# Kernel tuning notes

Measured on AMD Instinct MI355X. Metric: run time of the kernel, lower is better.

Reference implementation:

```python
import jax, jax.numpy as jnp
import numpy as np

# Model hyperparameters (from init_kwargs)
SIG = 10.0      # kernel length scale 'sig'
C = 0.0         # energy integration constant 'c'
STD = 1.0       # data std 'std'
N_ATOMS = 21    # aspirin-like molecule
T_ROWS = 12000  # n_train * n_perms (permutation-expanded training rows)
DESC = N_ATOMS * (N_ATOMS - 1) // 2  # 210
BATCH = 64


def setup_inputs() -> dict:
    key = jax.random.key(0)
    k1, k2, k3 = jax.random.split(key, 3)
    # Geometries: M x N x 3 Cartesian coordinates (spread out so atoms are distinct)
    Rs = jax.random.normal(k1, (BATCH, N_ATOMS, 3), dtype=jnp.float32) * 2.0
    # Permutation-expanded training descriptors (inverse distances -> positive)
    xs_train = jax.random.uniform(k2, (T_ROWS, DESC), dtype=jnp.float32, minval=0.05, maxval=1.0)
    Jx_alphas = jax.random.normal(k3, (T_ROWS, DESC), dtype=jnp.float32)
    return {"Rs": Rs, "xs_train": xs_train, "Jx_alphas": Jx_alphas}


def reference(Rs, xs_train, Jx_alphas):
    sig = SIG
    q = np.sqrt(5.0) / sig
    M, N, _ = Rs.shape
    i, j = np.tril_indices(N, k=-1)

    # Pairwise atomic displacement vectors and distances. Diagonal is padded with 1
    # (instead of inf as in the torch code) -- every diagonal contribution below is
    # multiplied by an exact zero (expand_tril zeroes the diagonal, diffs diag = 0),
    # so the value is irrelevant but this keeps gradients finite.
    diffs = Rs[:, :, None, :] - Rs[:, None, :, :]          # [M, N, N, 3]
    eye = jnp.eye(N, dtype=Rs.dtype)
    dists = jnp.sqrt(jnp.sum(diffs * diffs, axis=-1) + eye)  # [M, N, N]

    # Inverse-distance descriptor (strict lower triangle)
    xs = 1.0 / dists[:, i, j]                              # [M, DESC]

    # Descriptor-space differences vs all (permuted) training points
    x_diffs = (q * xs)[:, None, :] - q * xs_train[None]    # [M, T, DESC]
    x_dists = jnp.sqrt(jnp.sum(x_diffs * x_diffs, axis=-1))  # [M, T]

    # Matern-5/2 kernel pieces
    exp_xs = (5.0 / (3.0 * sig * sig)) * jnp.exp(-x_dists)   # [M, T]
    dot_x_diff_Jx = jnp.einsum('mtd,td->mt', x_diffs, Jx_alphas)  # [M, T]
    exp_xs_1_x_dists = exp_xs * (1.0 + x_dists)              # [M, T]

    # Descriptor-space force pieces
    F1s_x = jnp.einsum('mt,mtd->md', exp_xs * dot_x_diff_Jx, x_diffs)  # [M, DESC]
    F2s_x = exp_xs_1_x_dists @ Jx_alphas                               # [M, DESC]
    Fs_x = (F1s_x - F2s_x) * STD

    # expand_tril: scatter descriptor-space forces into symmetric NxN with zero diag
    full = jnp.zeros((M, N, N), dtype=Rs.dtype)
    full = full.at[:, i, j].set(Fs_x).at[:, j, i].set(Fs_x)

    # Cartesian forces: sum over first atom index (torch's .sum(dim=1))
    Fs = jnp.einsum('mab,mabk->mbk', full / dists ** 3, diffs)  # [M, N, 3]

    # Energies
    Es = jnp.sum(exp_xs_1_x_dists * dot_x_diff_Jx, axis=-1) / q
    Es = C + Es * STD
    return Es, Fs
```

## Files before the change

### kernel.cpp

```cpp
#include <hip/hip_runtime.h>
#include <hip/hip_fp16.h>
#include <math.h>

#define N_ATOMS 21
#define DESC 210
#define APAD 224
#define T_ROWS 12000
#define BATCH 64
#define NBLK_A 376
#define PCW 216

#define QCONST 0.22360679774997896f
#define K0CONST (1.0f/60.0f)

typedef short bf16x8 __attribute__((ext_vector_type(8)));
typedef float f32x4 __attribute__((ext_vector_type(4)));

__device__ __forceinline__ float u2f(unsigned int u) {
    union { unsigned int u; float f; } x; x.u = u; return x.f;
}
__device__ __forceinline__ unsigned short f2bf(float f) {
    union { float f; unsigned int u; } x; x.f = f;
    unsigned int r = x.u + 0x7fffu + ((x.u >> 16) & 1u);
    return (unsigned short)(r >> 16);
}
__device__ __forceinline__ float bf2f(unsigned short h) {
    return u2f((unsigned int)h << 16);
}

__global__ __launch_bounds__(256) void k_prep(const float* __restrict__ Rs,
                                              unsigned short* __restrict__ Abf,
                                              float* __restrict__ na2) {
    int m = blockIdx.x;
    __shared__ float R[N_ATOMS * 3];
    __shared__ float red[256];
    int tid = threadIdx.x;
    if (tid < N_ATOMS * 3) R[tid] = Rs[m * N_ATOMS * 3 + tid];
    __syncthreads();
    float val = 0.f;
    if (tid < DESC) {
        int p = tid;
        int i = (int)((1.0f + sqrtf(1.0f + 8.0f * (float)p)) * 0.5f);
        while (i * (i - 1) / 2 > p) --i;
        while ((i + 1) * i / 2 <= p) ++i;
        int j = p - i * (i - 1) / 2;
        float dx = R[i * 3 + 0] - R[j * 3 + 0];
        float dy = R[i * 3 + 1] - R[j * 3 + 1];
        float dz = R[i * 3 + 2] - R[j * 3 + 2];
        float d = sqrtf(dx * dx + dy * dy + dz * dz);
        val = QCONST / d;
    }
    unsigned short h = f2bf(val);
    if (tid < APAD) Abf[m * APAD + tid] = h;
    float va = bf2f(h);
    red[tid] = va * va;
    __syncthreads();
    for (int s = 128; s > 0; s >>= 1) {
        if (tid < s) red[tid] += red[tid + s];
        __syncthreads();
    }
    if (tid == 0) na2[m] = red[0];
}

#define BS_OFF 0
#define JS_OFF 14848
#define XT_OFF 29696
#define W_OFF  61952
#define NB_OFF 71168
#define BJ_OFF 71296
#define NA_OFF 71424
#define LDS_SZ 71680

__global__ __launch_bounds__(256) void k_fused(const float* __restrict__ Btr,
                                               const float* __restrict__ Jx,
                                               const unsigned short* __restrict__ Abf,
                                               const float* __restrict__ na2,
                                               float* __restrict__ es_p,
                                               float* __restrict__ rs_p,
                                               __half* __restrict__ pC) {
    __shared__ char lds[LDS_SZ];
    const int blk = blockIdx.x;
    const int t0 = blk * 32;
    const int tid = threadIdx.x;
    const int lane = tid & 63;
    const int w = __builtin_amdgcn_readfirstlane(tid >> 6);
    const int lr = lane & 15;
    const int kb = lane >> 4;

    uint4 au[7];
    {
        const unsigned short* ap = Abf + (w * 16 + lr) * APAD + kb * 8;
#pragma unroll
        for (int k8 = 0; k8 < 7; k8++) au[k8] = *(const uint4*)(ap + k8 * 32);
    }
    if (tid < 64) *(float*)(lds + NA_OFF + tid * 4) = na2[tid];

    {
        const int g = tid >> 3, gl = tid & 7;
        int tr = t0 + g; if (tr > T_ROWS - 1) tr = T_ROWS - 1;
        const float* bp = Btr + (size_t)tr * DESC;
        const float* jp = Jx + (size_t)tr * DESC;
        float nb = 0.f, bj = 0.f;
#pragma unroll
        for (int it = 0; it < 15; it++) {
            int c = it * 8 + gl;
            if (c < 116) {
                float2 vb = make_float2(0.f, 0.f), vj = make_float2(0.f, 0.f);
                if (c < 105) {
                    vb = *(const float2*)(bp + 2 * c);
                    vj = *(const float2*)(jp + 2 * c);
                }
                unsigned short hbx = f2bf(vb.x), hby = f2bf(vb.y);
                unsigned short hjx = f2bf(vj.x), hjy = f2bf(vj.y);
                *(unsigned int*)(lds + BS_OFF + g * 464 + c * 4) = (unsigned)hbx | ((unsigned)hby << 16);
                *(unsigned int*)(lds + JS_OFF + g * 464 + c * 4) = (unsigned)hjx | ((unsigned)hjy << 16);
                if (c < 112) {
                    const int d = 2 * c;
                    *(unsigned short*)(lds + XT_OFF + d * 144 + g * 2) = hbx;
                    *(unsigned short*)(lds + XT_OFF + (d + 1) * 144 + g * 2) = hby;
                    *(unsigned short*)(lds + XT_OFF + d * 144 + 64 + g * 2) = hjx;
                    *(unsigned short*)(lds + XT_OFF + (d + 1) * 144 + 64 + g * 2) = hjy;
                }
                float fbx = bf2f(hbx), fby = bf2f(hby);
                float fjx = bf2f(hjx), fjy = bf2f(hjy);
                nb = fmaf(fbx, fbx, nb); nb = fmaf(fby, fby, nb);
                bj = fmaf(fbx, fjx, bj); bj = fmaf(fby, fjy, bj);
            }
        }
#pragma unroll
        for (int m = 1; m < 8; m <<= 1) { nb += __shfl_xor(nb, m); bj += __shfl_xor(bj, m); }
        if (gl == 0) {
            *(float*)(lds + NB_OFF + g * 4) = nb;
            *(float*)(lds + BJ_OFF + g * 4) = bj;
        }
    }
    __syncthreads();

    f32x4 accP[2] = {{0.f,0.f,0.f,0.f},{0.f,0.f,0.f,0.f}};
    f32x4 accQ[2] = {{0.f,0.f,0.f,0.f},{0.f,0.f,0.f,0.f}};
#pragma unroll
    for (int k8 = 0; k8 < 7; k8++) {
        union { uint4 u; bf16x8 h; } a;
        a.u = au[k8];
#pragma unroll
        for (int nt = 0; nt < 2; nt++) {
            union { uint4 u; bf16x8 h; } bu, ju;
            const int ro = (nt * 16 + lr) * 464 + k8 * 64 + kb * 16;
            bu.u = *(const uint4*)(lds + BS_OFF + ro);
            ju.u = *(const uint4*)(lds + JS_OFF + ro);
            accP[nt] = __builtin_amdgcn_mfma_f32_16x16x32_bf16(a.h, bu.h, accP[nt], 0, 0, 0);
            accQ[nt] = __builtin_amdgcn_mfma_f32_16x16x32_bf16(a.h, ju.h, accQ[nt], 0, 0, 0);
        }
    }

    float na4[4];
#pragma unroll
    for (int r = 0; r < 4; r++)
        na4[r] = *(const float*)(lds + NA_OFF + (w * 16 + kb * 4 + r) * 4);
    float es4[4] = {0.f,0.f,0.f,0.f}, rs4[4] = {0.f,0.f,0.f,0.f};
#pragma unroll
    for (int nt = 0; nt < 2; nt++) {
        const int row = nt * 16 + lr;
        const float nb_c = *(const float*)(lds + NB_OFF + row * 4);
        const float bj_c = *(const float*)(lds + BJ_OFF + row * 4);
        const float msk = (t0 + row < T_ROWS) ? 1.f : 0.f;
#pragma unroll
        for (int r = 0; r < 4; r++) {
            float S = na4[r] + QCONST * QCONST * nb_c - 2.f * QCONST * accP[nt][r];
            float xd = sqrtf(fmaxf(S, 0.f));
            float e = K0CONST * __expf(-xd);
            float dot = (accQ[nt][r] - QCONST * bj_c) * msk;
            float w1 = e * dot;
            float w2 = e * (1.f + xd) * msk;
            es4[r] += w2 * dot; rs4[r] += w1;
            const int mrow = w * 16 + kb * 4 + r;
            *(unsigned short*)(lds + W_OFF + mrow * 144 + row * 2) = f2bf(QCONST * w1);
            *(unsigned short*)(lds + W_OFF + mrow * 144 + 64 + row * 2) = f2bf(w2);
        }
    }
#pragma unroll
    for (int m = 1; m < 16; m <<= 1) {
#pragma unroll
        for (int r = 0; r < 4; r++) {
            es4[r] += __shfl_xor(es4[r], m);
            rs4[r] += __shfl_xor(rs4[r], m);
        }
    }
    if (lr == 0) {
#pragma unroll
        for (int r = 0; r < 4; r++) {
            es_p[(size_t)(w * 16 + kb * 4 + r) * NBLK_A + blk] = es4[r];
            rs_p[(size_t)(w * 16 + kb * 4 + r) * NBLK_A + blk] = rs4[r];
        }
    }
    __syncthreads();

    {
        union { uint4 u; bf16x8 h; } wa0, wa1;
        const char* Wp = lds + W_OFF + (w * 16 + lr) * 144;
        wa0.u = *(const uint4*)(Wp + kb * 16);
        wa1.u = *(const uint4*)(Wp + 64 + kb * 16);
        __half* D = (__half*)lds;
#pragma unroll
        for (int dt = 0; dt < 14; dt++) {
            union { uint4 u; bf16x8 h; } xb0, xb1;
            const char* Xp = lds + XT_OFF + (dt * 16 + lr) * 144;
            xb0.u = *(const uint4*)(Xp + kb * 16);
            xb1.u = *(const uint4*)(Xp + 64 + kb * 16);
            f32x4 acc = {0.f, 0.f, 0.f, 0.f};
            acc = __builtin_amdgcn_mfma_f32_16x16x32_bf16(wa0.h, xb0.h, acc, 0, 0, 0);
            acc = __builtin_amdgcn_mfma_f32_16x16x32_bf16(wa1.h, xb1.h, acc, 0, 0, 0);
#pragma unroll
            for (int r = 0; r < 4; r++)
                D[(w * 16 + kb * 4 + r) * 224 + dt * 16 + lr] = __float2half(acc[r]);
        }
    }
    __syncthreads();

    {
        const char* D = (const char*)lds;
        for (int i = tid; i < 64 * 27; i += 256) {
            const int mrow = i / 27, oct = i % 27;
            uint4 v = *(const uint4*)(D + mrow * 448 + oct * 16);
            *(uint4*)((char*)pC + (((size_t)mrow * NBLK_A + blk) * PCW + oct * 8) * 2) = v;
        }
    }
}

__global__ __launch_bounds__(256) void k_final(const float* __restrict__ Rs,
                                               const unsigned short* __restrict__ Abf,
                                               const float* __restrict__ es_p,
                                               const float* __restrict__ rs_p,
                                               const __half* __restrict__ pC,
                                               float* __restrict__ out) {
    const int m = blockIdx.x;
    const int tid = threadIdx.x;
    __shared__ float parts[27][8][8];
    __shared__ float fsx[DESC];
    __shared__ float R[N_ATOMS * 3];
    __shared__ float s_rs, s_es;
    if (tid < N_ATOMS * 3) R[tid] = Rs[m * N_ATOMS * 3 + tid];
    if (tid < 216) {
        const int cg = tid / 27, o = tid % 27;
        float facc[8];
#pragma unroll
        for (int e = 0; e < 8; e++) facc[e] = 0.f;
        const __half* base = pC + (size_t)m * NBLK_A * PCW + o * 8;
#pragma unroll 4
        for (int c = cg; c < NBLK_A; c += 8) {
            uint4 v = *(const uint4*)(base + (size_t)c * PCW);
            const __half2* h = (const __half2*)&v;
#pragma unroll
            for (int p2 = 0; p2 < 4; p2++) {
                float2 f = __half22float2(h[p2]);
                facc[p2 * 2] += f.x;
                facc[p2 * 2 + 1] += f.y;
            }
        }
#pragma unroll
        for (int e = 0; e < 8; e++) parts[o][cg][e] = facc[e];
    }
    __syncthreads();
    if (tid < 64) {
        float es = 0.f, rs = 0.f;
        for (int c2 = tid; c2 < NBLK_A; c2 += 64) {
            es += es_p[(size_t)m * NBLK_A + c2];
            rs += rs_p[(size_t)m * NBLK_A + c2];
        }
        for (int mask = 1; mask < 64; mask <<= 1) {
            es += __shfl_xor(es, mask);
            rs += __shfl_xor(rs, mask);
        }
        if (tid == 0) { s_es = es; s_rs = rs; }
    }
    __syncthreads();
    if (tid < DESC) {
        float s = 0.f;
        const int o = tid >> 3, e = tid & 7;
#pragma unroll
        for (int cg = 0; cg < 8; cg++) s += parts[o][cg][e];
        fsx[tid] = s_rs * bf2f(Abf[m * APAD + tid]) - s;
    }
    if (tid == 0) out[m] = s_es * (1.0f / QCONST);
    __syncthreads();
    if (tid < N_ATOMS * 3) {
        int b = tid / 3, kk = tid % 3;
        float acc = 0.f;
        for (int a = 0; a < N_ATOMS; a++) {
            if (a == b) continue;
            float dx = R[a * 3 + 0] - R[b * 3 + 0];
            float dy = R[a * 3 + 1] - R[b * 3 + 1];
            float dz = R[a * 3 + 2] - R[b * 3 + 2];
            float d2 = dx * dx + dy * dy + dz * dz;
            float dist = sqrtf(d2);
            float inv3 = 1.0f / (d2 * dist);
            int hi = (a > b) ? a : b, lo = (a > b) ? b : a;
            int p = hi * (hi - 1) / 2 + lo;
            float diffk = (kk == 0) ? dx : ((kk == 1) ? dy : dz);
            acc = fmaf(fsx[p] * inv3, diffk, acc);
        }
        out[BATCH + m * N_ATOMS * 3 + tid] = acc;
    }
}

extern "C" void kernel_launch(void* const* d_in, const int* in_sizes, int n_in,
                              void* d_out, int out_size, void* d_ws, size_t ws_size,
                              hipStream_t stream) {
    (void)in_sizes; (void)n_in; (void)out_size; (void)ws_size;
    const float* Rs = (const float*)d_in[0];
    const float* Btr = (const float*)d_in[1];
    const float* Jx = (const float*)d_in[2];
    float* out = (float*)d_out;

    char* ws = (char*)d_ws;
    unsigned short* Abf = (unsigned short*)ws;  ws += (size_t)BATCH * APAD * 2;
    float* na2 = (float*)ws;                    ws += BATCH * 4;
    float* es_p = (float*)ws;                   ws += (size_t)BATCH * NBLK_A * 4;
    float* rs_p = (float*)ws;                   ws += (size_t)BATCH * NBLK_A * 4;
    __half* pC = (__half*)ws;

    k_prep<<<dim3(BATCH), dim3(256), 0, stream>>>(Rs, Abf, na2);
    k_fused<<<dim3(NBLK_A), dim3(256), 0, stream>>>(Btr, Jx, Abf, na2, es_p, rs_p, pC);
    k_final<<<dim3(BATCH), dim3(256), 0, stream>>>(Rs, Abf, es_p, rs_p, pC, out);
}
```

Before: 36.82 us.

## Use 24-row tiles over 500 blocks with batched loads and wider final reduction

Each block now handles 24 training rows instead of 32, so 12000 rows split evenly into 500 blocks with no tail masking. Global loads are issued as batched register arrays and split across threads by array (B vs J) before conversion. The norm and dot precomputation moves to a separate pass that reads back from LDS. The padded tile rows and columns are zeroed explicitly. The final reduction kernel uses 512 threads, with a separate warp summing the energy partials in parallel. More blocks give better CU coverage, but the MFMA padding wastes 8 of every 32 rows and there are more partials to reduce.

```diff
diff --git a/kernel.cpp b/kernel.cpp
--- a/kernel.cpp
+++ b/kernel.cpp
@@ -7,7 +7,8 @@
 #define APAD 224
 #define T_ROWS 12000
 #define BATCH 64
-#define NBLK_A 376
+#define NBLK 500
+#define TROWS_B 24
 #define PCW 216
 
 #define QCONST 0.22360679774997896f
@@ -80,61 +81,96 @@
                                                __half* __restrict__ pC) {
     __shared__ char lds[LDS_SZ];
     const int blk = blockIdx.x;
-    const int t0 = blk * 32;
+    const int t0 = blk * TROWS_B;
     const int tid = threadIdx.x;
     const int lane = tid & 63;
-    const int w = __builtin_amdgcn_readfirstlane(tid >> 6);
+    const int mt = __builtin_amdgcn_readfirstlane(tid >> 6);
     const int lr = lane & 15;
     const int kb = lane >> 4;
 
     uint4 au[7];
     {
-        const unsigned short* ap = Abf + (w * 16 + lr) * APAD + kb * 8;
+        const unsigned short* ap = Abf + (mt * 16 + lr) * APAD + kb * 8;
 #pragma unroll
         for (int k8 = 0; k8 < 7; k8++) au[k8] = *(const uint4*)(ap + k8 * 32);
     }
     if (tid < 64) *(float*)(lds + NA_OFF + tid * 4) = na2[tid];
 
     {
+        const uint4 z = make_uint4(0, 0, 0, 0);
+        for (int i = tid; i < 464; i += 256) {
+            const int arr = (i >= 232) ? 1 : 0;
+            const int j = i - arr * 232;
+            const int r = 24 + j / 29, c = j % 29;
+            *(uint4*)(lds + (arr ? JS_OFF : BS_OFF) + r * 464 + c * 16) = z;
+        }
+        for (int i = tid; i < 448; i += 256) {
+            const int d = i >> 1;
+            *(uint4*)(lds + XT_OFF + d * 144 + 96 + (i & 1) * 16) = z;
+        }
+        if (tid < 128) {
+            const int m = tid >> 1;
+            *(uint4*)(lds + W_OFF + m * 144 + 96 + (tid & 1) * 16) = z;
+        }
+        if (tid < 16)
+            *(float*)(lds + (tid < 8 ? NB_OFF : BJ_OFF) + (24 + (tid & 7)) * 4) = 0.f;
+    }
+
+#pragma unroll
+    for (int pass = 0; pass < 2; ++pass) {
+        if (pass == 1 && tid >= 128) break;
         const int g = tid >> 3, gl = tid & 7;
-        int tr = t0 + g; if (tr > T_ROWS - 1) tr = T_ROWS - 1;
-        const float* bp = Btr + (size_t)tr * DESC;
-        const float* jp = Jx + (size_t)tr * DESC;
+        int arr, row;
+        if (pass == 0) { arr = (g >= 24) ? 1 : 0; row = arr ? (g - 24) : g; }
+        else           { arr = 1; row = 8 + g; }
+        const float* sp = (arr ? Jx : Btr) + (size_t)(t0 + row) * DESC;
+        float2 v[14];
+#pragma unroll
+        for (int it = 0; it < 14; ++it) {
+            int c = it * 8 + gl; if (c > 104) c = 104;
+            v[it] = *(const float2*)(sp + 2 * c);
+        }
+        char* const rdst = lds + (arr ? JS_OFF : BS_OFF) + row * 464;
+        const int xtc = (arr ? 48 : 0) + row * 2;
+#pragma unroll
+        for (int it = 0; it < 14; ++it) {
+            const int c = it * 8 + gl;
+            const bool real = (c < 105);
+            const float2 vv = real ? v[it] : make_float2(0.f, 0.f);
+            const unsigned short hx = f2bf(vv.x), hy = f2bf(vv.y);
+            *(unsigned int*)(rdst + c * 4) = (unsigned)hx | ((unsigned)hy << 16);
+            if (real) {
+                const int d = 2 * c;
+                *(unsigned short*)(lds + XT_OFF + d * 144 + xtc) = hx;
+                *(unsigned short*)(lds + XT_OFF + (d + 1) * 144 + xtc) = hy;
+            }
+        }
+        if (gl < 4) *(unsigned int*)(rdst + (112 + gl) * 4) = 0u;
+    }
+    __syncthreads();
+
+    if (tid < 192) {
+        const int row = tid >> 3, gl = tid & 7;
         float nb = 0.f, bj = 0.f;
 #pragma unroll
-        for (int it = 0; it < 15; it++) {
-            int c = it * 8 + gl;
-            if (c < 116) {
-                float2 vb = make_float2(0.f, 0.f), vj = make_float2(0.f, 0.f);
-                if (c < 105) {
-                    vb = *(const float2*)(bp + 2 * c);
-                    vj = *(const float2*)(jp + 2 * c);
-                }
-                unsigned short hbx = f2bf(vb.x), hby = f2bf(vb.y);
-                unsigned short hjx = f2bf(vj.x), hjy = f2bf(vj.y);
-                *(unsigned int*)(lds + BS_OFF + g * 464 + c * 4) = (unsigned)hbx | ((unsigned)hby << 16);
-                *(unsigned int*)(lds + JS_OFF + g * 464 + c * 4) = (unsigned)hjx | ((unsigned)hjy << 16);
-                if (c < 112) {
-                    const int d = 2 * c;
-                    *(unsigned short*)(lds + XT_OFF + d * 144 + g * 2) = hbx;
-                    *(unsigned short*)(lds + XT_OFF + (d + 1) * 144 + g * 2) = hby;
-                    *(unsigned short*)(lds + XT_OFF + d * 144 + 64 + g * 2) = hjx;
-                    *(unsigned short*)(lds + XT_OFF + (d + 1) * 144 + 64 + g * 2) = hjy;
-                }
-                float fbx = bf2f(hbx), fby = bf2f(hby);
-                float fjx = bf2f(hjx), fjy = bf2f(hjy);
-                nb = fmaf(fbx, fbx, nb); nb = fmaf(fby, fby, nb);
-                bj = fmaf(fbx, fjx, bj); bj = fmaf(fby, fjy, bj);
-            }
-        }
-#pragma unroll
-        for (int m = 1; m < 8; m <<= 1) { nb += __shfl_xor(nb, m); bj += __shfl_xor(bj, m); }
+        for (int it = 0; it < 14; ++it) {
+            const int c = it * 8 + gl;
+            if (c < 105) {
+                const unsigned int ub = *(const unsigned int*)(lds + BS_OFF + row * 464 + c * 4);
+                const unsigned int uj = *(const unsigned int*)(lds + JS_OFF + row * 464 + c * 4);
+                const float bx = u2f(ub << 16), by = u2f(ub & 0xFFFF0000u);
+                const float jx2 = u2f(uj << 16), jy2 = u2f(uj & 0xFFFF0000u);
+                nb = fmaf(bx, bx, nb); nb = fmaf(by, by, nb);
+                bj = fmaf(bx, jx2, bj); bj = fmaf(by, jy2, bj);
+            }
+        }
+#pragma unroll
+        for (int msk = 1; msk < 8; msk <<= 1) { nb += __shfl_xor(nb, msk); bj += __shfl_xor(bj, msk); }
         if (gl == 0) {
-            *(float*)(lds + NB_OFF + g * 4) = nb;
-            *(float*)(lds + BJ_OFF + g * 4) = bj;
-        }
-    }
-    __syncthreads();
+            *(float*)(lds + NB_OFF + row * 4) = nb;
+            *(float*)(lds + BJ_OFF + row * 4) = bj;
+        }
+    }
 
     f32x4 accP[2] = {{0.f,0.f,0.f,0.f},{0.f,0.f,0.f,0.f}};
     f32x4 accQ[2] = {{0.f,0.f,0.f,0.f},{0.f,0.f,0.f,0.f}};
@@ -152,67 +188,70 @@
             accQ[nt] = __builtin_amdgcn_mfma_f32_16x16x32_bf16(a.h, ju.h, accQ[nt], 0, 0, 0);
         }
     }
+    __syncthreads();
 
     float na4[4];
 #pragma unroll
     for (int r = 0; r < 4; r++)
-        na4[r] = *(const float*)(lds + NA_OFF + (w * 16 + kb * 4 + r) * 4);
+        na4[r] = *(const float*)(lds + NA_OFF + (mt * 16 + kb * 4 + r) * 4);
     float es4[4] = {0.f,0.f,0.f,0.f}, rs4[4] = {0.f,0.f,0.f,0.f};
 #pragma unroll
     for (int nt = 0; nt < 2; nt++) {
         const int row = nt * 16 + lr;
         const float nb_c = *(const float*)(lds + NB_OFF + row * 4);
         const float bj_c = *(const float*)(lds + BJ_OFF + row * 4);
-        const float msk = (t0 + row < T_ROWS) ? 1.f : 0.f;
 #pragma unroll
         for (int r = 0; r < 4; r++) {
             float S = na4[r] + QCONST * QCONST * nb_c - 2.f * QCONST * accP[nt][r];
             float xd = sqrtf(fmaxf(S, 0.f));
             float e = K0CONST * __expf(-xd);
-            float dot = (accQ[nt][r] - QCONST * bj_c) * msk;
+            float dot = accQ[nt][r] - QCONST * bj_c;
             float w1 = e * dot;
-            float w2 = e * (1.f + xd) * msk;
+            float w2 = e * (1.f + xd);
             es4[r] += w2 * dot; rs4[r] += w1;
-            const int mrow = w * 16 + kb * 4 + r;
-            *(unsigned short*)(lds + W_OFF + mrow * 144 + row * 2) = f2bf(QCONST * w1);
-            *(unsigned short*)(lds + W_OFF + mrow * 144 + 64 + row * 2) = f2bf(w2);
-        }
-    }
-#pragma unroll
-    for (int m = 1; m < 16; m <<= 1) {
+            if (row < 24) {
+                const int mrow = mt * 16 + kb * 4 + r;
+                *(unsigned short*)(lds + W_OFF + mrow * 144 + row * 2) = f2bf(QCONST * w1);
+                *(unsigned short*)(lds + W_OFF + mrow * 144 + 48 + row * 2) = f2bf(w2);
+            }
+        }
+    }
+#pragma unroll
+    for (int msk = 1; msk < 16; msk <<= 1) {
 #pragma unroll
         for (int r = 0; r < 4; r++) {
-            es4[r] += __shfl_xor(es4[r], m);
-            rs4[r] += __shfl_xor(rs4[r], m);
+            es4[r] += __shfl_xor(es4[r], msk);
+            rs4[r] += __shfl_xor(rs4[r], msk);
         }
     }
     if (lr == 0) {
 #pragma unroll
         for (int r = 0; r < 4; r++) {
-            es_p[(size_t)(w * 16 + kb * 4 + r) * NBLK_A + blk] = es4[r];
-            rs_p[(size_t)(w * 16 + kb * 4 + r) * NBLK_A + blk] = rs4[r];
+            es_p[(size_t)(mt * 16 + kb * 4 + r) * NBLK + blk] = es4[r];
+            rs_p[(size_t)(mt * 16 + kb * 4 + r) * NBLK + blk] = rs4[r];
         }
     }
     __syncthreads();
 
     {
-        union { uint4 u; bf16x8 h; } wa0, wa1;
-        const char* Wp = lds + W_OFF + (w * 16 + lr) * 144;
-        wa0.u = *(const uint4*)(Wp + kb * 16);
-        wa1.u = *(const uint4*)(Wp + 64 + kb * 16);
+        union { uint4 u; bf16x8 h; } wa[2];
+        const char* Wp = lds + W_OFF + (mt * 16 + lr) * 144;
+#pragma unroll
+        for (int c = 0; c < 2; c++) wa[c].u = *(const uint4*)(Wp + c * 64 + kb * 16);
         __half* D = (__half*)lds;
 #pragma unroll
         for (int dt = 0; dt < 14; dt++) {
-            union { uint4 u; bf16x8 h; } xb0, xb1;
             const char* Xp = lds + XT_OFF + (dt * 16 + lr) * 144;
-            xb0.u = *(const uint4*)(Xp + kb * 16);
-            xb1.u = *(const uint4*)(Xp + 64 + kb * 16);
             f32x4 acc = {0.f, 0.f, 0.f, 0.f};
-            acc = __builtin_amdgcn_mfma_f32_16x16x32_bf16(wa0.h, xb0.h, acc, 0, 0, 0);
-            acc = __builtin_amdgcn_mfma_f32_16x16x32_bf16(wa1.h, xb1.h, acc, 0, 0, 0);
+#pragma unroll
+            for (int c = 0; c < 2; c++) {
+                union { uint4 u; bf16x8 h; } xb;
+                xb.u = *(const uint4*)(Xp + c * 64 + kb * 16);
+                acc = __builtin_amdgcn_mfma_f32_16x16x32_bf16(wa[c].h, xb.h, acc, 0, 0, 0);
+            }
 #pragma unroll
             for (int r = 0; r < 4; r++)
-                D[(w * 16 + kb * 4 + r) * 224 + dt * 16 + lr] = __float2half(acc[r]);
+                D[(mt * 16 + kb * 4 + r) * 224 + dt * 16 + lr] = __float2half(acc[r]);
         }
     }
     __syncthreads();
@@ -222,12 +261,12 @@
         for (int i = tid; i < 64 * 27; i += 256) {
             const int mrow = i / 27, oct = i % 27;
             uint4 v = *(const uint4*)(D + mrow * 448 + oct * 16);
-            *(uint4*)((char*)pC + (((size_t)mrow * NBLK_A + blk) * PCW + oct * 8) * 2) = v;
-        }
-    }
-}
-
-__global__ __launch_bounds__(256) void k_final(const float* __restrict__ Rs,
+            *(uint4*)((char*)pC + (((size_t)mrow * NBLK + blk) * PCW + oct * 8) * 2) = v;
+        }
+    }
+}
+
+__global__ __launch_bounds__(512) void k_final(const float* __restrict__ Rs,
                                                const unsigned short* __restrict__ Abf,
                                                const float* __restrict__ es_p,
                                                const float* __restrict__ rs_p,
@@ -235,19 +274,18 @@
                                                float* __restrict__ out) {
     const int m = blockIdx.x;
     const int tid = threadIdx.x;
-    __shared__ float parts[27][8][8];
+    __shared__ float parts[27][16][8];
     __shared__ float fsx[DESC];
     __shared__ float R[N_ATOMS * 3];
     __shared__ float s_rs, s_es;
     if (tid < N_ATOMS * 3) R[tid] = Rs[m * N_ATOMS * 3 + tid];
-    if (tid < 216) {
+    if (tid < 432) {
         const int cg = tid / 27, o = tid % 27;
         float facc[8];
 #pragma unroll
         for (int e = 0; e < 8; e++) facc[e] = 0.f;
-        const __half* base = pC + (size_t)m * NBLK_A * PCW + o * 8;
-#pragma unroll 4
-        for (int c = cg; c < NBLK_A; c += 8) {
+        const __half* base = pC + (size_t)m * NBLK * PCW + o * 8;
+        for (int c = cg; c < NBLK; c += 16) {
             uint4 v = *(const uint4*)(base + (size_t)c * PCW);
             const __half2* h = (const __half2*)&v;
 #pragma unroll
@@ -259,32 +297,31 @@
         }
 #pragma unroll
         for (int e = 0; e < 8; e++) parts[o][cg][e] = facc[e];
-    }
-    __syncthreads();
-    if (tid < 64) {
+    } else if (tid >= 448) {
+        const int lx = tid - 448;
         float es = 0.f, rs = 0.f;
-        for (int c2 = tid; c2 < NBLK_A; c2 += 64) {
-            es += es_p[(size_t)m * NBLK_A + c2];
-            rs += rs_p[(size_t)m * NBLK_A + c2];
-        }
-        for (int mask = 1; mask < 64; mask <<= 1) {
-            es += __shfl_xor(es, mask);
-            rs += __shfl_xor(rs, mask);
-        }
-        if (tid == 0) { s_es = es; s_rs = rs; }
+        for (int c2 = lx; c2 < NBLK; c2 += 64) {
+            es += es_p[(size_t)m * NBLK + c2];
+            rs += rs_p[(size_t)m * NBLK + c2];
+        }
+        for (int msk = 1; msk < 64; msk <<= 1) {
+            es += __shfl_xor(es, msk);
+            rs += __shfl_xor(rs, msk);
+        }
+        if (lx == 0) { s_es = es; s_rs = rs; }
     }
     __syncthreads();
     if (tid < DESC) {
         float s = 0.f;
         const int o = tid >> 3, e = tid & 7;
 #pragma unroll
-        for (int cg = 0; cg < 8; cg++) s += parts[o][cg][e];
+        for (int cg = 0; cg < 16; cg++) s += parts[o][cg][e];
         fsx[tid] = s_rs * bf2f(Abf[m * APAD + tid]) - s;
     }
     if (tid == 0) out[m] = s_es * (1.0f / QCONST);
     __syncthreads();
     if (tid < N_ATOMS * 3) {
-        int b = tid / 3, kk = tid % 3;
+        const int b = tid / 3, kk = tid % 3;
         float acc = 0.f;
         for (int a = 0; a < N_ATOMS; a++) {
             if (a == b) continue;
@@ -315,11 +352,11 @@
     char* ws = (char*)d_ws;
     unsigned short* Abf = (unsigned short*)ws;  ws += (size_t)BATCH * APAD * 2;
     float* na2 = (float*)ws;                    ws += BATCH * 4;
-    float* es_p = (float*)ws;                   ws += (size_t)BATCH * NBLK_A * 4;
-    float* rs_p = (float*)ws;                   ws += (size_t)BATCH * NBLK_A * 4;
+    float* es_p = (float*)ws;                   ws += (size_t)BATCH * NBLK * 4;
+    float* rs_p = (float*)ws;                   ws += (size_t)BATCH * NBLK * 4;
     __half* pC = (__half*)ws;
 
     k_prep<<<dim3(BATCH), dim3(256), 0, stream>>>(Rs, Abf, na2);
-    k_fused<<<dim3(NBLK_A), dim3(256), 0, stream>>>(Btr, Jx, Abf, na2, es_p, rs_p, pC);
-    k_final<<<dim3(BATCH), dim3(256), 0, stream>>>(Rs, Abf, es_p, rs_p, pC, out);
-}
+    k_fused<<<dim3(NBLK), dim3(256), 0, stream>>>(Btr, Jx, Abf, na2, es_p, rs_p, pC);
+    k_final<<<dim3(BATCH), dim3(512), 0, stream>>>(Rs, Abf, es_p, rs_p, pC, out);
+}
```

After: 42.13 us. 1.14x slower.
